# Kernel optimization log

Hardware: AMD Instinct MI355X
Metric: run time of the kernel (lower is better)

Reference implementation:

```python
import jax, jax.numpy as jnp
import numpy as np

DIM = 384
NUM_HEADS = 12
WS = 8            # window_size
SS = 4            # shift_size
HEAD_DIM = DIM // NUM_HEADS
SCALE = HEAD_DIM ** -0.5
N = WS * WS       # tokens per window
EPS = 1e-5
MLP_HIDDEN = 4 * DIM

# relative position index (static, matches torch buffer construction)
_coords = np.stack(np.meshgrid(np.arange(WS), np.arange(WS), indexing='ij')).reshape(2, -1)
_rel = (_coords[:, :, None] - _coords[:, None, :]).transpose(1, 2, 0)  # [N,N,2]
_rel[..., 0] += WS - 1
_rel[..., 1] += WS - 1
_rel[..., 0] *= 2 * WS - 1
RPI = jnp.asarray(_rel.sum(-1))  # [N,N] int


def layer_norm(x, g, b):
    m = x.mean(-1, keepdims=True)
    v = ((x - m) ** 2).mean(-1, keepdims=True)
    return (x - m) / jnp.sqrt(v + EPS) * g + b


def window_partition(x):
    B, Hh, Ww, C = x.shape
    x = x.reshape(B, Hh // WS, WS, Ww // WS, WS, C).transpose(0, 1, 3, 2, 4, 5)
    return x.reshape(-1, WS, WS, C)


def window_reverse(w, Hh, Ww):
    B = w.shape[0] // ((Hh // WS) * (Ww // WS))
    x = w.reshape(B, Hh // WS, Ww // WS, WS, WS, -1).transpose(0, 1, 3, 2, 4, 5)
    return x.reshape(B, Hh, Ww, -1)


def attention_mask(Hp, Wp):
    # region id along each axis: 0 = [0, Hp-WS), 1 = [Hp-WS, Hp-SS), 2 = [Hp-SS, Hp)
    h_id = np.zeros(Hp, np.int32); h_id[Hp - WS:Hp - SS] = 1; h_id[Hp - SS:] = 2
    w_id = np.zeros(Wp, np.int32); w_id[Wp - WS:Wp - SS] = 1; w_id[Wp - SS:] = 2
    cnt = h_id[:, None] * 3 + w_id[None, :]                      # [Hp, Wp]
    img = jnp.asarray(cnt, jnp.float32).reshape(1, Hp, Wp, 1)
    mw = window_partition(img).reshape(-1, N)                    # [nW, N]
    am = mw[:, None, :] - mw[:, :, None]                         # [nW, N, N]
    return jnp.where(am != 0, jnp.float32(-100.0), jnp.float32(0.0))


def setup_inputs() -> dict:
    key = jax.random.key(0)
    ks = jax.random.split(key, 8)
    B, H, W = 32, 64, 64
    std = 0.02
    return {
        'x': jax.random.normal(ks[0], (B, H * W, DIM), jnp.float32),
        'qkv_w': jax.random.normal(ks[1], (DIM, 3 * DIM), jnp.float32) * std,
        'qkv_b': jnp.zeros((3 * DIM,), jnp.float32),
        'proj_w': jax.random.normal(ks[2], (DIM, DIM), jnp.float32) * std,
        'proj_b': jnp.zeros((DIM,), jnp.float32),
        'rpb_table': jax.random.normal(ks[3], ((2 * WS - 1) * (2 * WS - 1), NUM_HEADS), jnp.float32) * std,
        'n1_g': jnp.ones((DIM,), jnp.float32), 'n1_b': jnp.zeros((DIM,), jnp.float32),
        'n2_g': jnp.ones((DIM,), jnp.float32), 'n2_b': jnp.zeros((DIM,), jnp.float32),
        'fc1_w': jax.random.normal(ks[4], (DIM, MLP_HIDDEN), jnp.float32) * std,
        'fc1_b': jnp.zeros((MLP_HIDDEN,), jnp.float32),
        'fc2_w': jax.random.normal(ks[5], (MLP_HIDDEN, DIM), jnp.float32) * std,
        'fc2_b': jnp.zeros((DIM,), jnp.float32),
        'H': 64, 'W': 64,
    }


def reference(x, qkv_w, qkv_b, proj_w, proj_b, rpb_table, n1_g, n1_b, n2_g, n2_b,
              fc1_w, fc1_b, fc2_w, fc2_b, H, W):
    B, L, C = x.shape
    shortcut = x
    h = layer_norm(x, n1_g, n1_b).reshape(B, H, W, C)
    pad_r = (WS - W % WS) % WS
    pad_b = (WS - H % WS) % WS
    if pad_r or pad_b:
        h = jnp.pad(h, ((0, 0), (0, pad_b), (0, pad_r), (0, 0)))
    Hp, Wp = H + pad_b, W + pad_r
    shifted = jnp.roll(h, shift=(-SS, -SS), axis=(1, 2))
    xw = window_partition(shifted).reshape(-1, N, C)             # [B_, N, C]
    B_ = xw.shape[0]

    qkv = (xw @ qkv_w + qkv_b).reshape(B_, N, 3, NUM_HEADS, HEAD_DIM)
    q = qkv[:, :, 0].transpose(0, 2, 1, 3) * SCALE               # [B_, h, N, d]
    k = qkv[:, :, 1].transpose(0, 2, 1, 3)
    v = qkv[:, :, 2].transpose(0, 2, 1, 3)

    attn = jnp.einsum('bhnd,bhmd->bhnm', q, k)                   # [B_, h, N, N]
    bias = rpb_table[RPI].transpose(2, 0, 1)                     # [h, N, N]
    attn = attn + bias[None]

    mask = attention_mask(Hp, Wp)                                # [nW, N, N]
    nW = mask.shape[0]
    attn = attn.reshape(B_ // nW, nW, NUM_HEADS, N, N) + mask[None, :, None]
    attn = jax.nn.softmax(attn.reshape(B_, NUM_HEADS, N, N), axis=-1)

    out = jnp.einsum('bhnm,bhmd->bhnd', attn, v)
    out = out.transpose(0, 2, 1, 3).reshape(B_, N, C)
    out = out @ proj_w + proj_b

    out = window_reverse(out.reshape(-1, WS, WS, C), Hp, Wp)
    out = jnp.roll(out, shift=(SS, SS), axis=(1, 2))
    out = out[:, :H, :W, :].reshape(B, H * W, C)

    x = shortcut + out
    h2 = layer_norm(x, n2_g, n2_b)
    mlp = jax.nn.gelu(h2 @ fc1_w + fc1_b, approximate=False) @ fc2_w + fc2_b
    return x + mlp
```

## Files before the change

### kernel.cpp

```cpp
#include <hip/hip_runtime.h>
#include <math.h>


#define ROWS_TOTAL 131072
#define NWIN_TOTAL 2048

typedef __attribute__((ext_vector_type(8))) __bf16 bf16x8;
typedef __attribute__((ext_vector_type(4))) float f32x4;
typedef __attribute__((ext_vector_type(8))) unsigned short ushort8;

__device__ __forceinline__ unsigned short f2bf(float f) {
  unsigned u = __builtin_bit_cast(unsigned, f);
  u = (u + 0x7fffu + ((u >> 16) & 1u)) >> 16;
  return (unsigned short)u;
}
__device__ __forceinline__ float bf2f(unsigned short u) {
  return __builtin_bit_cast(float, (unsigned)u << 16);
}

__device__ __forceinline__ void gload16(const void* g, void* l) {
  __builtin_amdgcn_global_load_lds(
      (const __attribute__((address_space(1))) unsigned int*)g,
      (__attribute__((address_space(3))) unsigned int*)l, 16, 0, 0);
}

__device__ __forceinline__ int gather_row(int win, int t) {
  int b = win >> 6, wi = (win >> 3) & 7, wj = win & 7;
  int gi = (wi * 8 + (t >> 3) + 4) & 63;
  int gj = (wj * 8 + (t & 7) + 4) & 63;
  return (b << 12) + (gi << 6) + gj;
}

__device__ __forceinline__ float gelu_f(float v) {
  float x = v * 0.70710678118654752f;
  float ax = fabsf(x);
  float t = 1.f / (1.f + 0.3275911f * ax);
  float poly =
      t * (0.254829592f +
           t * (-0.284496736f +
                t * (1.421413741f + t * (-1.453152027f + t * 1.061405429f))));
  float er = 1.f - poly * __expf(-x * x);
  er = copysignf(er, x);
  return 0.5f * v * (1.f + er);
}

#define VM4() asm volatile("s_waitcnt vmcnt(4)" ::: "memory")
#define VM0() asm volatile("s_waitcnt vmcnt(0)" ::: "memory")
#define ABAR() asm volatile("s_barrier" ::: "memory")

#define STGA_(buf_, kt_, c_)                                          \
  gload16(aSrcC[c_] + (size_t)(kt_) * 64,                             \
          (char*)As + (buf_) * 32768 + (c_) * 8192 + w * 1024)
#define STGB_(buf_, kt_, c_)                                          \
  gload16(bSrcC[c_] + (size_t)(kt_) * 64,                             \
          (char*)Bs + (buf_) * 24576 + (c_) * 8192 + w * 1024)

#define GEMM_DECLS()                                                  \
  f32x4 acc[8][3];                                                    \
  _Pragma("unroll") for (int i_ = 0; i_ < 8; ++i_)                    \
  _Pragma("unroll") for (int j_ = 0; j_ < 3; ++j_)                    \
      acc[i_][j_] = (f32x4)(0.f);                                     \
  const int sl0 = ((hi) ^ (lr & 7)) * 8;                              \
  const int sl1 = ((4 + hi) ^ (lr & 7)) * 8;                          \
  const int aB0 = (wr * 128 + lr) * 64 + sl0;                         \
  const int aB1 = (wr * 128 + lr) * 64 + sl1;                         \
  const int bB0 = (wc * 48 + lr) * 64 + sl0;                          \
  const int bB1 = (wc * 48 + lr) * 64 + sl1;

#define GEMM_CORE(NT_)                                                \
  {                                                                   \
    STGA_(0, 0, 0); STGA_(0, 0, 1); STGA_(0, 0, 2); STGA_(0, 0, 3);   \
    STGB_(0, 0, 0); STGB_(0, 0, 1); STGB_(0, 0, 2);                   \
    STGA_(1, 1, 0); STGA_(1, 1, 1); STGA_(1, 1, 2); STGA_(1, 1, 3);   \
    VM4(); ABAR();                                                    \
    int curA = 0;                                                     \
    for (int t = 0; t < (NT_); ++t) {                                 \
      const int curB = t & 1;                                         \
      const ushort* AsC = (const ushort*)As + curA * 16384;           \
      const ushort* BsC = (const ushort*)Bs + curB * 12288;           \
      if (t + 1 < (NT_)) {                                            \
        STGB_(curB ^ 1, t + 1, 0);                                    \
        STGB_(curB ^ 1, t + 1, 1);                                    \
        STGB_(curB ^ 1, t + 1, 2);                                    \
      }                                                               \
      if (t + 2 < (NT_)) {                                            \
        int nbA = curA + 2; if (nbA >= 3) nbA -= 3;                   \
        STGA_(nbA, t + 2, 0); STGA_(nbA, t + 2, 1);                   \
        STGA_(nbA, t + 2, 2); STGA_(nbA, t + 2, 3);                   \
      }                                                               \
      bf16x8 bv0[3], bv1[3];                                          \
      _Pragma("unroll") for (int nj = 0; nj < 3; ++nj) {              \
        bv0[nj] = *(const bf16x8*)(BsC + bB0 + nj * 1024);            \
        bv1[nj] = *(const bf16x8*)(BsC + bB1 + nj * 1024);            \
      }                                                               \
      _Pragma("unroll") for (int mi = 0; mi < 8; ++mi) {              \
        bf16x8 a0 = *(const bf16x8*)(AsC + aB0 + mi * 1024);          \
        bf16x8 a1 = *(const bf16x8*)(AsC + aB1 + mi * 1024);          \
        _Pragma("unroll") for (int nj = 0; nj < 3; ++nj) {            \
          acc[mi][nj] = __builtin_amdgcn_mfma_f32_16x16x32_bf16(      \
              a0, bv0[nj], acc[mi][nj], 0, 0, 0);                     \
          acc[mi][nj] = __builtin_amdgcn_mfma_f32_16x16x32_bf16(      \
              a1, bv1[nj], acc[mi][nj], 0, 0, 0);                     \
        }                                                             \
      }                                                               \
      if (t + 2 < (NT_)) { VM4(); ABAR(); }                           \
      else if (t + 1 < (NT_)) { VM0(); ABAR(); }                      \
      ++curA; if (curA == 3) curA = 0;                                \
    }                                                                 \
  }

#define GRID_SWZ(NP_)                                                 \
  int p, bm;                                                          \
  {                                                                   \
    int lin = blockIdx.y * (NP_) + blockIdx.x;                        \
    if ((gridDim.y & 7) == 0) {                                       \
      int xcd = lin & 7, q = lin >> 3;                                \
      p = q % (NP_); bm = (q / (NP_)) * 8 + xcd;                      \
    } else { p = blockIdx.x; bm = blockIdx.y; }                       \
  }

__global__ __launch_bounds__(256) void wprep_k(
    const float* __restrict__ qkvw, const float* __restrict__ projw,
    const float* __restrict__ fc1w, const float* __restrict__ fc2w,
    ushort* __restrict__ wq, ushort* __restrict__ wp,
    ushort* __restrict__ w1, ushort* __restrict__ w2) {
  int gid = blockIdx.x * 256 + threadIdx.x;
  const int S1 = 1152 * 384;
  const int S2 = S1 + 384 * 384;
  const int S3 = S2 + 1536 * 384;
  const int S4 = S3 + 384 * 1536;
  if (gid < S1) {
    int n = gid / 384, k = gid - n * 384;
    wq[gid] = f2bf(qkvw[(size_t)k * 1152 + n]);
  } else if (gid < S2) {
    int i = gid - S1, n = i / 384, k = i - n * 384;
    wp[i] = f2bf(projw[(size_t)k * 384 + n]);
  } else if (gid < S3) {
    int i = gid - S2, n = i / 384, k = i - n * 384;
    w1[i] = f2bf(fc1w[(size_t)k * 1536 + n]);
  } else if (gid < S4) {
    int i = gid - S3, n = i / 1536, k = i - n * 1536;
    w2[i] = f2bf(fc2w[(size_t)k * 384 + n]);
  }
}

__global__ __launch_bounds__(256) void ln_fused_k(
    const float* __restrict__ x, const float* __restrict__ g,
    const float* __restrict__ b, ushort* __restrict__ o) {
  int wid = threadIdx.x >> 6, lane = threadIdx.x & 63;
  int row = (blockIdx.x << 2) + wid;
  const float* p = x + (size_t)row * 384;
  float2 v[3];
  float s = 0.f, ss = 0.f;
#pragma unroll
  for (int c = 0; c < 3; ++c) {
    v[c] = *(const float2*)(p + lane * 2 + c * 128);
    s += v[c].x + v[c].y;
    ss += v[c].x * v[c].x + v[c].y * v[c].y;
  }
#pragma unroll
  for (int off = 1; off < 64; off <<= 1) {
    s += __shfl_xor(s, off);
    ss += __shfl_xor(ss, off);
  }
  float m = s * (1.f / 384.f);
  float r = rsqrtf(ss * (1.f / 384.f) - m * m + 1e-5f);
  ushort* op = o + (size_t)row * 384;
#pragma unroll
  for (int c = 0; c < 3; ++c) {
    float2 gg = *(const float2*)(g + lane * 2 + c * 128);
    float2 bb = *(const float2*)(b + lane * 2 + c * 128);
    union { ushort u[2]; unsigned w; } pk;
    pk.u[0] = f2bf((v[c].x - m) * r * gg.x + bb.x);
    pk.u[1] = f2bf((v[c].y - m) * r * gg.y + bb.y);
    *(unsigned*)(op + lane * 2 + c * 128) = pk.w;
  }
}

__global__ __launch_bounds__(512, 2) void qkv_mfma_k(
    const ushort* __restrict__ xln, const ushort* __restrict__ wq,
    const float* __restrict__ qkvb, ushort* __restrict__ qkvd, int wc0) {
  __shared__ __align__(16) ushort As[3][16384];
  __shared__ __align__(16) ushort Bs[2][12288];
  const int tid = threadIdx.x;
  const int w = tid >> 6, lane = tid & 63;
  const int wr = w >> 2, wc = w & 3;
  const int lr = lane & 15, hi = lane >> 4;
  GRID_SWZ(6);
  const int n0 = p * 192;
  const int sg = ((tid & 7) ^ ((tid >> 3) & 7)) * 8;
  const ushort* aSrcC[4];
  const ushort* bSrcC[3];
#pragma unroll
  for (int c = 0; c < 4; ++c)
    aSrcC[c] =
        xln + (size_t)gather_row(wc0 + bm * 4 + c, tid >> 3) * 384 + sg;
#pragma unroll
  for (int c = 0; c < 3; ++c)
    bSrcC[c] = wq + (size_t)(n0 + c * 64 + (tid >> 3)) * 384 + sg;
  GEMM_DECLS();
  GEMM_CORE(6);
  const float scale = 0.17677669529663687f;
#pragma unroll
  for (int mi = 0; mi < 8; ++mi) {
#pragma unroll
    for (int r = 0; r < 4; ++r) {
      int rr = wr * 128 + mi * 16 + (hi << 2) + r;
      size_t row = (size_t)(bm * 256 + rr);
#pragma unroll
      for (int nj = 0; nj < 3; ++nj) {
        int nc = n0 + wc * 48 + nj * 16 + lr;
        float v = acc[mi][nj][r] + qkvb[nc];
        if (nc < 384) v *= scale;
        qkvd[row * 1152 + nc] = f2bf(v);
      }
    }
  }
}

__global__ __launch_bounds__(128) void attn_k(
    const ushort* __restrict__ qkv, const float* __restrict__ rpb,
    ushort* __restrict__ ao, int wc0) {
  __shared__ __align__(16) float kbuf[2][64][32];
  __shared__ __align__(16) float vbuf[2][64][32];
  __shared__ float bias[2][232];
  __shared__ int region[64];
  const int tid = threadIdx.x;
  const int wid = tid >> 6, lane = tid & 63;
  const int w = blockIdx.x, win = wc0 + w;
  const int head = blockIdx.y * 2 + wid;
  if (tid < 64) {
    int wi = (win >> 3) & 7, wj = win & 7;
    int pi = wi * 8 + (tid >> 3), pj = wj * 8 + (tid & 7);
    int ri = pi < 56 ? 0 : (pi < 60 ? 1 : 2);
    int rj = pj < 56 ? 0 : (pj < 60 ? 1 : 2);
    region[tid] = ri * 3 + rj;
  }
  const ushort* base = qkv + (size_t)(w * 64) * 1152;
  const int kcol = 384 + head * 32, vcol = 768 + head * 32;
#pragma unroll
  for (int s = 0; s < 4; ++s) {
    int f = s * 64 + lane;
    int r = f >> 2, c = (f & 3) * 8;
    ushort8 ku = *(const ushort8*)(base + (size_t)r * 1152 + kcol + c);
    ushort8 vu = *(const ushort8*)(base + (size_t)r * 1152 + vcol + c);
#pragma unroll
    for (int j = 0; j < 8; ++j) {
      kbuf[wid][r][c + j] = bf2f(ku[j]);
      vbuf[wid][r][c + j] = bf2f(vu[j]);
    }
  }
  for (int s = lane; s < 225; s += 64) bias[wid][s] = rpb[s * 12 + head];
  __syncthreads();
  const int i = lane;
  float qr[32];
  const ushort* qp = base + (size_t)i * 1152 + head * 32;
#pragma unroll
  for (int c = 0; c < 4; ++c) {
    ushort8 qu = *(const ushort8*)(qp + c * 8);
#pragma unroll
    for (int j = 0; j < 8; ++j) qr[c * 8 + j] = bf2f(qu[j]);
  }
  const int yi = i >> 3, xi = i & 7, regi = region[i];
  float sc[64];
  float mx = -3.0e38f;
#pragma unroll
  for (int j = 0; j < 64; ++j) {
    float a = 0.f;
#pragma unroll
    for (int c = 0; c < 32; c += 4) {
      float4 kv = *(float4*)&kbuf[wid][j][c];
      a = fmaf(qr[c], kv.x, a);
      a = fmaf(qr[c + 1], kv.y, a);
      a = fmaf(qr[c + 2], kv.z, a);
      a = fmaf(qr[c + 3], kv.w, a);
    }
    int dy = yi - (j >> 3) + 7, dx = xi - (j & 7) + 7;
    a += bias[wid][dy * 15 + dx];
    if (region[j] != regi) a -= 100.f;
    sc[j] = a;
    mx = fmaxf(mx, a);
  }
  float sum = 0.f;
#pragma unroll
  for (int j = 0; j < 64; ++j) {
    float e = __expf(sc[j] - mx);
    sc[j] = e;
    sum += e;
  }
  const float inv = 1.f / sum;
  float o[32];
#pragma unroll
  for (int c = 0; c < 32; ++c) o[c] = 0.f;
#pragma unroll
  for (int j = 0; j < 64; ++j) {
    float p = sc[j];
#pragma unroll
    for (int c = 0; c < 32; c += 4) {
      float4 vv = *(float4*)&vbuf[wid][j][c];
      o[c] = fmaf(p, vv.x, o[c]);
      o[c + 1] = fmaf(p, vv.y, o[c + 1]);
      o[c + 2] = fmaf(p, vv.z, o[c + 2]);
      o[c + 3] = fmaf(p, vv.w, o[c + 3]);
    }
  }
  ushort* op = ao + ((size_t)(w * 64 + i)) * 384 + (head << 5);
#pragma unroll
  for (int c = 0; c < 32; c += 8) {
    ushort8 pk;
#pragma unroll
    for (int j2 = 0; j2 < 8; ++j2) pk[j2] = f2bf(o[c + j2] * inv);
    *(ushort8*)(op + c) = pk;
  }
}

__global__ __launch_bounds__(512, 2) void proj_mfma_k(
    const ushort* __restrict__ ao, const ushort* __restrict__ wp,
    const float* __restrict__ pb, const float* __restrict__ x,
    float* __restrict__ x2, int wc0) {
  __shared__ __align__(16) ushort As[3][16384];
  __shared__ __align__(16) ushort Bs[2][12288];
  const int tid = threadIdx.x;
  const int w = tid >> 6, lane = tid & 63;
  const int wr = w >> 2, wc = w & 3;
  const int lr = lane & 15, hi = lane >> 4;
  GRID_SWZ(2);
  const int n0 = p * 192;
  const int sg = ((tid & 7) ^ ((tid >> 3) & 7)) * 8;
  const ushort* aSrcC[4];
  const ushort* bSrcC[3];
#pragma unroll
  for (int c = 0; c < 4; ++c)
    aSrcC[c] = ao + (size_t)(bm * 256 + c * 64 + (tid >> 3)) * 384 + sg;
#pragma unroll
  for (int c = 0; c < 3; ++c)
    bSrcC[c] = wp + (size_t)(n0 + c * 64 + (tid >> 3)) * 384 + sg;
  GEMM_DECLS();
  GEMM_CORE(6);
#pragma unroll
  for (int mi = 0; mi < 8; ++mi) {
#pragma unroll
    for (int r = 0; r < 4; ++r) {
      int rr = wr * 128 + mi * 16 + (hi << 2) + r;
      int gl = bm * 256 + rr;
      int gr = gather_row(wc0 + (gl >> 6), gl & 63);
#pragma unroll
      for (int nj = 0; nj < 3; ++nj) {
        int nc = n0 + wc * 48 + nj * 16 + lr;
        size_t idx = (size_t)gr * 384 + nc;
        x2[idx] = acc[mi][nj][r] + pb[nc] + x[idx];
      }
    }
  }
}

__global__ __launch_bounds__(512, 2) void fc1_mfma_k(
    const ushort* __restrict__ x2ln, const ushort* __restrict__ w1,
    const float* __restrict__ fb, ushort* __restrict__ hm, int row0) {
  __shared__ __align__(16) ushort As[3][16384];
  __shared__ __align__(16) ushort Bs[2][12288];
  const int tid = threadIdx.x;
  const int w = tid >> 6, lane = tid & 63;
  const int wr = w >> 2, wc = w & 3;
  const int lr = lane & 15, hi = lane >> 4;
  GRID_SWZ(8);
  const int n0 = p * 192;
  const int sg = ((tid & 7) ^ ((tid >> 3) & 7)) * 8;
  const ushort* aSrcC[4];
  const ushort* bSrcC[3];
#pragma unroll
  for (int c = 0; c < 4; ++c)
    aSrcC[c] =
        x2ln + (size_t)(row0 + bm * 256 + c * 64 + (tid >> 3)) * 384 + sg;
#pragma unroll
  for (int c = 0; c < 3; ++c)
    bSrcC[c] = w1 + (size_t)(n0 + c * 64 + (tid >> 3)) * 384 + sg;
  GEMM_DECLS();
  GEMM_CORE(6);
#pragma unroll
  for (int mi = 0; mi < 8; ++mi) {
#pragma unroll
    for (int r = 0; r < 4; ++r) {
      int rr = wr * 128 + mi * 16 + (hi << 2) + r;
      size_t lrow = (size_t)(bm * 256 + rr);
#pragma unroll
      for (int nj = 0; nj < 3; ++nj) {
        int nc = n0 + wc * 48 + nj * 16 + lr;
        float v = gelu_f(acc[mi][nj][r] + fb[nc]);
        hm[lrow * 1536 + nc] = f2bf(v);
      }
    }
  }
}

__global__ __launch_bounds__(512, 2) void fc2_mfma_k(
    const ushort* __restrict__ hm, const ushort* __restrict__ w2,
    const float* __restrict__ fb, float* __restrict__ out, int row0) {
  __shared__ __align__(16) ushort As[3][16384];
  __shared__ __align__(16) ushort Bs[2][12288];
  const int tid = threadIdx.x;
  const int w = tid >> 6, lane = tid & 63;
  const int wr = w >> 2, wc = w & 3;
  const int lr = lane & 15, hi = lane >> 4;
  GRID_SWZ(2);
  const int n0 = p * 192;
  const int sg = ((tid & 7) ^ ((tid >> 3) & 7)) * 8;
  const ushort* aSrcC[4];
  const ushort* bSrcC[3];
#pragma unroll
  for (int c = 0; c < 4; ++c)
    aSrcC[c] = hm + (size_t)(bm * 256 + c * 64 + (tid >> 3)) * 1536 + sg;
#pragma unroll
  for (int c = 0; c < 3; ++c)
    bSrcC[c] = w2 + (size_t)(n0 + c * 64 + (tid >> 3)) * 1536 + sg;
  GEMM_DECLS();
  GEMM_CORE(24);
#pragma unroll
  for (int mi = 0; mi < 8; ++mi) {
#pragma unroll
    for (int r = 0; r < 4; ++r) {
      int rr = wr * 128 + mi * 16 + (hi << 2) + r;
      size_t grow = (size_t)(row0 + bm * 256 + rr);
#pragma unroll
      for (int nj = 0; nj < 3; ++nj) {
        int nc = n0 + wc * 48 + nj * 16 + lr;
        size_t idx = grow * 384 + nc;
        out[idx] = out[idx] + acc[mi][nj][r] + fb[nc];
      }
    }
  }
}

extern "C" void kernel_launch(void* const* d_in, const int* in_sizes, int n_in,
                              void* d_out, int out_size, void* d_ws, size_t ws_size,
                              hipStream_t stream) {
  const float* x = (const float*)d_in[0];
  const float* qkv_w = (const float*)d_in[1];
  const float* qkv_b = (const float*)d_in[2];
  const float* proj_w = (const float*)d_in[3];
  const float* proj_b = (const float*)d_in[4];
  const float* rpb = (const float*)d_in[5];
  const float* n1g = (const float*)d_in[6];
  const float* n1b = (const float*)d_in[7];
  const float* n2g = (const float*)d_in[8];
  const float* n2b = (const float*)d_in[9];
  const float* fc1w = (const float*)d_in[10];
  const float* fc1b = (const float*)d_in[11];
  const float* fc2w = (const float*)d_in[12];
  const float* fc2b = (const float*)d_in[13];
  float* out = (float*)d_out;
  char* ws = (char*)d_ws;

  ushort* wq = (ushort*)ws;
  ushort* wp = wq + 442368;
  ushort* w1 = wp + 147456;
  ushort* w2 = w1 + 589824;
  ushort* xln = (ushort*)(ws + 3538944);
  char* scratch = ws + 3538944 + 100663296;
  size_t base = 3538944 + 100663296;
  size_t ssz = (ws_size > base) ? ws_size - base : 0;

  wprep_k<<<6912, 256, 0, stream>>>(qkv_w, proj_w, fc1w, fc2w, wq, wp, w1, w2);
  ln_fused_k<<<ROWS_TOTAL / 4, 256, 0, stream>>>(x, n1g, n1b, xln);

  const size_t perwin = 196608;
  int nwc = (int)(ssz / perwin);
  if (nwc > NWIN_TOTAL) nwc = NWIN_TOTAL;
  nwc &= ~31;
  if (nwc < 32) nwc = 32;
  ushort* qkvd = (ushort*)scratch;
  ushort* ao = qkvd + (size_t)nwc * 73728;
  for (int wc0 = 0; wc0 < NWIN_TOTAL; wc0 += nwc) {
    int nw = (NWIN_TOTAL - wc0 < nwc) ? (NWIN_TOTAL - wc0) : nwc;
    qkv_mfma_k<<<dim3(6, nw / 4), 512, 0, stream>>>(xln, wq, qkv_b, qkvd, wc0);
    attn_k<<<dim3(nw, 6), 128, 0, stream>>>(qkvd, rpb, ao, wc0);
    proj_mfma_k<<<dim3(2, nw / 4), 512, 0, stream>>>(ao, wp, proj_b, x, out,
                                                     wc0);
  }

  ln_fused_k<<<ROWS_TOTAL / 4, 256, 0, stream>>>(out, n2g, n2b, xln);
  const size_t pergrp = 786432;
  int ngc = (int)(ssz / pergrp);
  if (ngc > 512) ngc = 512;
  ngc &= ~7;
  if (ngc < 8) ngc = 8;
  ushort* hm = (ushort*)scratch;
  for (int g0 = 0; g0 < 512; g0 += ngc) {
    int ng = (512 - g0 < ngc) ? (512 - g0) : ngc;
    fc1_mfma_k<<<dim3(8, ng), 512, 0, stream>>>(xln, w1, fc1b, hm, g0 * 256);
    fc2_mfma_k<<<dim3(2, ng), 512, 0, stream>>>(hm, w2, fc2b, out, g0 * 256);
  }
}
```

Before: 1.549 ms.

## Use weight-resident persistent GEMM kernels for QKV, proj and FC1

Replaces the QKV, projection and FC1 GEMMs with persistent 256-thread kernels. Each block keeps a 48-column weight panel (full K=384) resident in LDS and loops over 256-row M tiles with a stride of the grid height, double-buffering only the activation tiles. The aim is to stop re-streaming weight tiles for every output tile and to overlap the next tile's A load with the current epilogue. In exchange, per-block tiles are smaller (256x48) and the grid is capped, which may reduce MFMA density and occupancy. FC2 keeps its original kernel with the macros inlined.

```diff
diff --git a/kernel.cpp b/kernel.cpp
--- a/kernel.cpp
+++ b/kernel.cpp
@@ -48,75 +48,44 @@
 #define VM0() asm volatile("s_waitcnt vmcnt(0)" ::: "memory")
 #define ABAR() asm volatile("s_barrier" ::: "memory")
 
-#define STGA_(buf_, kt_, c_)                                          \
-  gload16(aSrcC[c_] + (size_t)(kt_) * 64,                             \
-          (char*)As + (buf_) * 32768 + (c_) * 8192 + w * 1024)
-#define STGB_(buf_, kt_, c_)                                          \
-  gload16(bSrcC[c_] + (size_t)(kt_) * 64,                             \
-          (char*)Bs + (buf_) * 24576 + (c_) * 8192 + w * 1024)
-
-#define GEMM_DECLS()                                                  \
-  f32x4 acc[8][3];                                                    \
-  _Pragma("unroll") for (int i_ = 0; i_ < 8; ++i_)                    \
-  _Pragma("unroll") for (int j_ = 0; j_ < 3; ++j_)                    \
-      acc[i_][j_] = (f32x4)(0.f);                                     \
-  const int sl0 = ((hi) ^ (lr & 7)) * 8;                              \
-  const int sl1 = ((4 + hi) ^ (lr & 7)) * 8;                          \
-  const int aB0 = (wr * 128 + lr) * 64 + sl0;                         \
-  const int aB1 = (wr * 128 + lr) * 64 + sl1;                         \
-  const int bB0 = (wc * 48 + lr) * 64 + sl0;                          \
-  const int bB1 = (wc * 48 + lr) * 64 + sl1;
-
-#define GEMM_CORE(NT_)                                                \
-  {                                                                   \
-    STGA_(0, 0, 0); STGA_(0, 0, 1); STGA_(0, 0, 2); STGA_(0, 0, 3);   \
-    STGB_(0, 0, 0); STGB_(0, 0, 1); STGB_(0, 0, 2);                   \
-    STGA_(1, 1, 0); STGA_(1, 1, 1); STGA_(1, 1, 2); STGA_(1, 1, 3);   \
-    VM4(); ABAR();                                                    \
-    int curA = 0;                                                     \
-    for (int t = 0; t < (NT_); ++t) {                                 \
-      const int curB = t & 1;                                         \
-      const ushort* AsC = (const ushort*)As + curA * 16384;           \
-      const ushort* BsC = (const ushort*)Bs + curB * 12288;           \
-      if (t + 1 < (NT_)) {                                            \
-        STGB_(curB ^ 1, t + 1, 0);                                    \
-        STGB_(curB ^ 1, t + 1, 1);                                    \
-        STGB_(curB ^ 1, t + 1, 2);                                    \
-      }                                                               \
-      if (t + 2 < (NT_)) {                                            \
-        int nbA = curA + 2; if (nbA >= 3) nbA -= 3;                   \
-        STGA_(nbA, t + 2, 0); STGA_(nbA, t + 2, 1);                   \
-        STGA_(nbA, t + 2, 2); STGA_(nbA, t + 2, 3);                   \
-      }                                                               \
-      bf16x8 bv0[3], bv1[3];                                          \
-      _Pragma("unroll") for (int nj = 0; nj < 3; ++nj) {              \
-        bv0[nj] = *(const bf16x8*)(BsC + bB0 + nj * 1024);            \
-        bv1[nj] = *(const bf16x8*)(BsC + bB1 + nj * 1024);            \
-      }                                                               \
-      _Pragma("unroll") for (int mi = 0; mi < 8; ++mi) {              \
-        bf16x8 a0 = *(const bf16x8*)(AsC + aB0 + mi * 1024);          \
-        bf16x8 a1 = *(const bf16x8*)(AsC + aB1 + mi * 1024);          \
-        _Pragma("unroll") for (int nj = 0; nj < 3; ++nj) {            \
-          acc[mi][nj] = __builtin_amdgcn_mfma_f32_16x16x32_bf16(      \
-              a0, bv0[nj], acc[mi][nj], 0, 0, 0);                     \
-          acc[mi][nj] = __builtin_amdgcn_mfma_f32_16x16x32_bf16(      \
-              a1, bv1[nj], acc[mi][nj], 0, 0, 0);                     \
-        }                                                             \
-      }                                                               \
-      if (t + 2 < (NT_)) { VM4(); ABAR(); }                           \
-      else if (t + 1 < (NT_)) { VM0(); ABAR(); }                      \
-      ++curA; if (curA == 3) curA = 0;                                \
-    }                                                                 \
-  }
-
-#define GRID_SWZ(NP_)                                                 \
-  int p, bm;                                                          \
-  {                                                                   \
-    int lin = blockIdx.y * (NP_) + blockIdx.x;                        \
-    if ((gridDim.y & 7) == 0) {                                       \
-      int xcd = lin & 7, q = lin >> 3;                                \
-      p = q % (NP_); bm = (q / (NP_)) * 8 + xcd;                      \
-    } else { p = blockIdx.x; bm = blockIdx.y; }                       \
+#define WSTG_A(buf_, kt_)                                               \
+  _Pragma("unroll") for (int c_ = 0; c_ < 4; ++c_)                      \
+      gload16(aSrc[c_] + (size_t)(kt_) * 64,                            \
+              (char*)As + (buf_) * 16384 + (c_ * 256 + tid) * 16);
+
+#define WGEMM_PRO()                                                     \
+  _Pragma("unroll") for (int i_ = 0; i_ < 9; ++i_) {                    \
+    int id_ = i_ * 256 + tid;                                           \
+    int row_ = id_ / 48, g_ = id_ - row_ * 48;                          \
+    gload16((const char*)bpan + (size_t)row_ * 768 +                    \
+                ((g_ ^ (row_ & 7)) << 4),                               \
+            (char*)Bres + id_ * 16);                                    \
+  }                                                                     \
+  int aOff[4], bRow[3];                                                 \
+  _Pragma("unroll") for (int mi_ = 0; mi_ < 4; ++mi_)                   \
+      aOff[mi_] = (w * 64 + mi_ * 16 + lr) * 64 +                       \
+                  ((hi ^ ((lr >> 1) & 3)) << 4);                        \
+  _Pragma("unroll") for (int nj_ = 0; nj_ < 3; ++nj_)                   \
+      bRow[nj_] = (nj_ * 16 + lr) * 768;                                \
+  const int sg = (((tid & 3) ^ ((tid >> 3) & 3)) << 4);
+
+#define WGEMM_STEP(t_, stage_, STAGE_EXPR)                              \
+  {                                                                     \
+    STAGE_EXPR;                                                         \
+    const int bslot = ((((t_) << 2) + hi) ^ (lr & 7)) << 4;             \
+    bf16x8 bv[3];                                                       \
+    _Pragma("unroll") for (int nj = 0; nj < 3; ++nj)                    \
+        bv[nj] = *(const bf16x8*)((char*)Bres + bRow[nj] + bslot);      \
+    _Pragma("unroll") for (int mi = 0; mi < 4; ++mi) {                  \
+      bf16x8 av =                                                       \
+          *(const bf16x8*)((char*)As + buf * 16384 + aOff[mi]);         \
+      _Pragma("unroll") for (int nj = 0; nj < 3; ++nj)                  \
+          acc[mi][nj] = __builtin_amdgcn_mfma_f32_16x16x32_bf16(        \
+              av, bv[nj], acc[mi][nj], 0, 0, 0);                        \
+    }                                                                   \
+    if (stage_) { VM4(); } else { VM0(); }                              \
+    ABAR();                                                             \
+    buf ^= 1;                                                           \
   }
 
 __global__ __launch_bounds__(256) void wprep_k(
@@ -177,45 +146,68 @@
   }
 }
 
-__global__ __launch_bounds__(512, 2) void qkv_mfma_k(
+__global__ __launch_bounds__(256) void qkv_wres_k(
     const ushort* __restrict__ xln, const ushort* __restrict__ wq,
-    const float* __restrict__ qkvb, ushort* __restrict__ qkvd, int wc0) {
-  __shared__ __align__(16) ushort As[3][16384];
-  __shared__ __align__(16) ushort Bs[2][12288];
+    const float* __restrict__ qkvb, ushort* __restrict__ qkvd, int wc0,
+    int NMT, int G) {
+  __shared__ __align__(16) ushort Bres[2304 * 8];
+  __shared__ __align__(16) ushort As[2][8192];
   const int tid = threadIdx.x;
-  const int w = tid >> 6, lane = tid & 63;
-  const int wr = w >> 2, wc = w & 3;
+  const int lane = tid & 63, w = tid >> 6;
   const int lr = lane & 15, hi = lane >> 4;
-  GRID_SWZ(6);
-  const int n0 = p * 192;
-  const int sg = ((tid & 7) ^ ((tid >> 3) & 7)) * 8;
-  const ushort* aSrcC[4];
-  const ushort* bSrcC[3];
-#pragma unroll
-  for (int c = 0; c < 4; ++c)
-    aSrcC[c] =
-        xln + (size_t)gather_row(wc0 + bm * 4 + c, tid >> 3) * 384 + sg;
-#pragma unroll
-  for (int c = 0; c < 3; ++c)
-    bSrcC[c] = wq + (size_t)(n0 + c * 64 + (tid >> 3)) * 384 + sg;
-  GEMM_DECLS();
-  GEMM_CORE(6);
+  const int p = blockIdx.x, n0 = p * 48;
+  const ushort* bpan = wq + (size_t)n0 * 384;
+  int mt = (int)blockIdx.y;
+  if (mt >= NMT) return;
+  WGEMM_PRO();
+  const char* aSrc[4];
+#define QKV_SETA(mt_)                                                   \
+  _Pragma("unroll") for (int c = 0; c < 4; ++c) {                       \
+    int rowc = (mt_) * 256 + c * 64 + (tid >> 2);                       \
+    aSrc[c] = (const char*)xln +                                        \
+              (size_t)gather_row(wc0 + (rowc >> 6), rowc & 63) * 768 +  \
+              sg;                                                       \
+  }
+  QKV_SETA(mt);
+  WSTG_A(0, 0);
+  VM0();
+  ABAR();
+  int buf = 0;
   const float scale = 0.17677669529663687f;
-#pragma unroll
-  for (int mi = 0; mi < 8; ++mi) {
-#pragma unroll
-    for (int r = 0; r < 4; ++r) {
-      int rr = wr * 128 + mi * 16 + (hi << 2) + r;
-      size_t row = (size_t)(bm * 256 + rr);
-#pragma unroll
-      for (int nj = 0; nj < 3; ++nj) {
-        int nc = n0 + wc * 48 + nj * 16 + lr;
-        float v = acc[mi][nj][r] + qkvb[nc];
-        if (nc < 384) v *= scale;
-        qkvd[row * 1152 + nc] = f2bf(v);
-      }
-    }
-  }
+  while (true) {
+    int nextmt = mt + G;
+    bool last = (nextmt >= NMT);
+    f32x4 acc[4][3];
+#pragma unroll
+    for (int i_ = 0; i_ < 4; ++i_)
+#pragma unroll
+      for (int j_ = 0; j_ < 3; ++j_) acc[i_][j_] = (f32x4)(0.f);
+    for (int t = 0; t < 11; ++t) {
+      WGEMM_STEP(t, true, WSTG_A(buf ^ 1, t + 1));
+    }
+    if (!last) {
+      WGEMM_STEP(11, true, { QKV_SETA(nextmt); WSTG_A(buf ^ 1, 0); });
+    } else {
+      WGEMM_STEP(11, false, {});
+    }
+#pragma unroll
+    for (int mi = 0; mi < 4; ++mi) {
+#pragma unroll
+      for (int r = 0; r < 4; ++r) {
+        size_t row = (size_t)(mt * 256 + w * 64 + mi * 16 + (hi << 2) + r);
+#pragma unroll
+        for (int nj = 0; nj < 3; ++nj) {
+          int nc = n0 + nj * 16 + lr;
+          float v = acc[mi][nj][r] + qkvb[nc];
+          if (nc < 384) v *= scale;
+          qkvd[row * 1152 + nc] = f2bf(v);
+        }
+      }
+    }
+    if (last) break;
+    mt = nextmt;
+  }
+#undef QKV_SETA
 }
 
 __global__ __launch_bounds__(128) void attn_k(
@@ -314,84 +306,133 @@
   }
 }
 
-__global__ __launch_bounds__(512, 2) void proj_mfma_k(
+__global__ __launch_bounds__(256) void proj_wres_k(
     const ushort* __restrict__ ao, const ushort* __restrict__ wp,
     const float* __restrict__ pb, const float* __restrict__ x,
-    float* __restrict__ x2, int wc0) {
-  __shared__ __align__(16) ushort As[3][16384];
-  __shared__ __align__(16) ushort Bs[2][12288];
+    float* __restrict__ x2, int wc0, int NMT, int G) {
+  __shared__ __align__(16) ushort Bres[2304 * 8];
+  __shared__ __align__(16) ushort As[2][8192];
   const int tid = threadIdx.x;
-  const int w = tid >> 6, lane = tid & 63;
-  const int wr = w >> 2, wc = w & 3;
+  const int lane = tid & 63, w = tid >> 6;
   const int lr = lane & 15, hi = lane >> 4;
-  GRID_SWZ(2);
-  const int n0 = p * 192;
-  const int sg = ((tid & 7) ^ ((tid >> 3) & 7)) * 8;
-  const ushort* aSrcC[4];
-  const ushort* bSrcC[3];
-#pragma unroll
-  for (int c = 0; c < 4; ++c)
-    aSrcC[c] = ao + (size_t)(bm * 256 + c * 64 + (tid >> 3)) * 384 + sg;
-#pragma unroll
-  for (int c = 0; c < 3; ++c)
-    bSrcC[c] = wp + (size_t)(n0 + c * 64 + (tid >> 3)) * 384 + sg;
-  GEMM_DECLS();
-  GEMM_CORE(6);
-#pragma unroll
-  for (int mi = 0; mi < 8; ++mi) {
-#pragma unroll
-    for (int r = 0; r < 4; ++r) {
-      int rr = wr * 128 + mi * 16 + (hi << 2) + r;
-      int gl = bm * 256 + rr;
-      int gr = gather_row(wc0 + (gl >> 6), gl & 63);
-#pragma unroll
-      for (int nj = 0; nj < 3; ++nj) {
-        int nc = n0 + wc * 48 + nj * 16 + lr;
-        size_t idx = (size_t)gr * 384 + nc;
-        x2[idx] = acc[mi][nj][r] + pb[nc] + x[idx];
-      }
-    }
-  }
-}
-
-__global__ __launch_bounds__(512, 2) void fc1_mfma_k(
+  const int p = blockIdx.x, n0 = p * 48;
+  const ushort* bpan = wp + (size_t)n0 * 384;
+  int mt = (int)blockIdx.y;
+  if (mt >= NMT) return;
+  WGEMM_PRO();
+  const char* aSrc[4];
+#define PROJ_SETA(mt_)                                                  \
+  _Pragma("unroll") for (int c = 0; c < 4; ++c)                         \
+      aSrc[c] = (const char*)ao +                                       \
+                (size_t)((mt_) * 256 + c * 64 + (tid >> 2)) * 768 + sg;
+  PROJ_SETA(mt);
+  WSTG_A(0, 0);
+  VM0();
+  ABAR();
+  int buf = 0;
+  while (true) {
+    int nextmt = mt + G;
+    bool last = (nextmt >= NMT);
+    f32x4 acc[4][3];
+#pragma unroll
+    for (int i_ = 0; i_ < 4; ++i_)
+#pragma unroll
+      for (int j_ = 0; j_ < 3; ++j_) acc[i_][j_] = (f32x4)(0.f);
+    for (int t = 0; t < 11; ++t) {
+      WGEMM_STEP(t, true, WSTG_A(buf ^ 1, t + 1));
+    }
+    if (!last) {
+      WGEMM_STEP(11, true, { PROJ_SETA(nextmt); WSTG_A(buf ^ 1, 0); });
+    } else {
+      WGEMM_STEP(11, false, {});
+    }
+#pragma unroll
+    for (int mi = 0; mi < 4; ++mi) {
+#pragma unroll
+      for (int r = 0; r < 4; ++r) {
+        int gl = mt * 256 + w * 64 + mi * 16 + (hi << 2) + r;
+        int gr = gather_row(wc0 + (gl >> 6), gl & 63);
+#pragma unroll
+        for (int nj = 0; nj < 3; ++nj) {
+          int nc = n0 + nj * 16 + lr;
+          size_t idx = (size_t)gr * 384 + nc;
+          x2[idx] = acc[mi][nj][r] + pb[nc] + x[idx];
+        }
+      }
+    }
+    if (last) break;
+    mt = nextmt;
+  }
+#undef PROJ_SETA
+}
+
+__global__ __launch_bounds__(256) void fc1_wres_k(
     const ushort* __restrict__ x2ln, const ushort* __restrict__ w1,
-    const float* __restrict__ fb, ushort* __restrict__ hm, int row0) {
-  __shared__ __align__(16) ushort As[3][16384];
-  __shared__ __align__(16) ushort Bs[2][12288];
+    const float* __restrict__ fb, ushort* __restrict__ hm, int row0,
+    int NMT, int G) {
+  __shared__ __align__(16) ushort Bres[2304 * 8];
+  __shared__ __align__(16) ushort As[2][8192];
   const int tid = threadIdx.x;
-  const int w = tid >> 6, lane = tid & 63;
-  const int wr = w >> 2, wc = w & 3;
+  const int lane = tid & 63, w = tid >> 6;
   const int lr = lane & 15, hi = lane >> 4;
-  GRID_SWZ(8);
-  const int n0 = p * 192;
-  const int sg = ((tid & 7) ^ ((tid >> 3) & 7)) * 8;
-  const ushort* aSrcC[4];
-  const ushort* bSrcC[3];
-#pragma unroll
-  for (int c = 0; c < 4; ++c)
-    aSrcC[c] =
-        x2ln + (size_t)(row0 + bm * 256 + c * 64 + (tid >> 3)) * 384 + sg;
-#pragma unroll
-  for (int c = 0; c < 3; ++c)
-    bSrcC[c] = w1 + (size_t)(n0 + c * 64 + (tid >> 3)) * 384 + sg;
-  GEMM_DECLS();
-  GEMM_CORE(6);
-#pragma unroll
-  for (int mi = 0; mi < 8; ++mi) {
-#pragma unroll
-    for (int r = 0; r < 4; ++r) {
-      int rr = wr * 128 + mi * 16 + (hi << 2) + r;
-      size_t lrow = (size_t)(bm * 256 + rr);
-#pragma unroll
-      for (int nj = 0; nj < 3; ++nj) {
-        int nc = n0 + wc * 48 + nj * 16 + lr;
-        float v = gelu_f(acc[mi][nj][r] + fb[nc]);
-        hm[lrow * 1536 + nc] = f2bf(v);
-      }
-    }
-  }
-}
+  const int p = blockIdx.x, n0 = p * 48;
+  const ushort* bpan = w1 + (size_t)n0 * 384;
+  int mt = (int)blockIdx.y;
+  if (mt >= NMT) return;
+  WGEMM_PRO();
+  const char* aSrc[4];
+#define FC1_SETA(mt_)                                                   \
+  _Pragma("unroll") for (int c = 0; c < 4; ++c)                         \
+      aSrc[c] = (const char*)x2ln +                                     \
+                (size_t)(row0 + (mt_) * 256 + c * 64 + (tid >> 2)) *    \
+                    768 +                                               \
+                sg;
+  FC1_SETA(mt);
+  WSTG_A(0, 0);
+  VM0();
+  ABAR();
+  int buf = 0;
+  while (true) {
+    int nextmt = mt + G;
+    bool last = (nextmt >= NMT);
+    f32x4 acc[4][3];
+#pragma unroll
+    for (int i_ = 0; i_ < 4; ++i_)
+#pragma unroll
+      for (int j_ = 0; j_ < 3; ++j_) acc[i_][j_] = (f32x4)(0.f);
+    for (int t = 0; t < 11; ++t) {
+      WGEMM_STEP(t, true, WSTG_A(buf ^ 1, t + 1));
+    }
+    if (!last) {
+      WGEMM_STEP(11, true, { FC1_SETA(nextmt); WSTG_A(buf ^ 1, 0); });
+    } else {
+      WGEMM_STEP(11, false, {});
+    }
+#pragma unroll
+    for (int mi = 0; mi < 4; ++mi) {
+#pragma unroll
+      for (int r = 0; r < 4; ++r) {
+        size_t lrow = (size_t)(mt * 256 + w * 64 + mi * 16 + (hi << 2) + r);
+#pragma unroll
+        for (int nj = 0; nj < 3; ++nj) {
+          int nc = n0 + nj * 16 + lr;
+          float v = gelu_f(acc[mi][nj][r] + fb[nc]);
+          hm[lrow * 1536 + nc] = f2bf(v);
+        }
+      }
+    }
+    if (last) break;
+    mt = nextmt;
+  }
+#undef FC1_SETA
+}
+
+#define STGA2_(buf_, kt_, c_)                                         \
+  gload16(aSrcC[c_] + (size_t)(kt_) * 64,                             \
+          (char*)As + (buf_) * 32768 + (c_) * 8192 + w * 1024)
+#define STGB2_(buf_, kt_, c_)                                         \
+  gload16(bSrcC[c_] + (size_t)(kt_) * 64,                             \
+          (char*)Bs + (buf_) * 24576 + (c_) * 8192 + w * 1024)
 
 __global__ __launch_bounds__(512, 2) void fc2_mfma_k(
     const ushort* __restrict__ hm, const ushort* __restrict__ w2,
@@ -402,19 +443,78 @@
   const int w = tid >> 6, lane = tid & 63;
   const int wr = w >> 2, wc = w & 3;
   const int lr = lane & 15, hi = lane >> 4;
-  GRID_SWZ(2);
+  int p, bm;
+  {
+    int lin = blockIdx.y * 2 + blockIdx.x;
+    if ((gridDim.y & 7) == 0) {
+      int xcd = lin & 7, q = lin >> 3;
+      p = q % 2; bm = (q / 2) * 8 + xcd;
+    } else { p = blockIdx.x; bm = blockIdx.y; }
+  }
   const int n0 = p * 192;
-  const int sg = ((tid & 7) ^ ((tid >> 3) & 7)) * 8;
+  const int sg2 = ((tid & 7) ^ ((tid >> 3) & 7)) * 8;
   const ushort* aSrcC[4];
   const ushort* bSrcC[3];
 #pragma unroll
   for (int c = 0; c < 4; ++c)
-    aSrcC[c] = hm + (size_t)(bm * 256 + c * 64 + (tid >> 3)) * 1536 + sg;
+    aSrcC[c] = hm + (size_t)(bm * 256 + c * 64 + (tid >> 3)) * 1536 + sg2;
 #pragma unroll
   for (int c = 0; c < 3; ++c)
-    bSrcC[c] = w2 + (size_t)(n0 + c * 64 + (tid >> 3)) * 1536 + sg;
-  GEMM_DECLS();
-  GEMM_CORE(24);
+    bSrcC[c] = w2 + (size_t)(n0 + c * 64 + (tid >> 3)) * 1536 + sg2;
+  f32x4 acc[8][3];
+#pragma unroll
+  for (int i_ = 0; i_ < 8; ++i_)
+#pragma unroll
+    for (int j_ = 0; j_ < 3; ++j_) acc[i_][j_] = (f32x4)(0.f);
+  const int sl0 = ((hi) ^ (lr & 7)) * 8;
+  const int sl1 = ((4 + hi) ^ (lr & 7)) * 8;
+  const int aB0 = (wr * 128 + lr) * 64 + sl0;
+  const int aB1 = (wr * 128 + lr) * 64 + sl1;
+  const int bB0 = (wc * 48 + lr) * 64 + sl0;
+  const int bB1 = (wc * 48 + lr) * 64 + sl1;
+  {
+    STGA2_(0, 0, 0); STGA2_(0, 0, 1); STGA2_(0, 0, 2); STGA2_(0, 0, 3);
+    STGB2_(0, 0, 0); STGB2_(0, 0, 1); STGB2_(0, 0, 2);
+    STGA2_(1, 1, 0); STGA2_(1, 1, 1); STGA2_(1, 1, 2); STGA2_(1, 1, 3);
+    VM4(); ABAR();
+    int curA = 0;
+    for (int t = 0; t < 24; ++t) {
+      const int curB = t & 1;
+      const ushort* AsC = (const ushort*)As + curA * 16384;
+      const ushort* BsC = (const ushort*)Bs + curB * 12288;
+      if (t + 1 < 24) {
+        STGB2_(curB ^ 1, t + 1, 0);
+        STGB2_(curB ^ 1, t + 1, 1);
+        STGB2_(curB ^ 1, t + 1, 2);
+      }
+      if (t + 2 < 24) {
+        int nbA = curA + 2; if (nbA >= 3) nbA -= 3;
+        STGA2_(nbA, t + 2, 0); STGA2_(nbA, t + 2, 1);
+        STGA2_(nbA, t + 2, 2); STGA2_(nbA, t + 2, 3);
+      }
+      bf16x8 bv0[3], bv1[3];
+#pragma unroll
+      for (int nj = 0; nj < 3; ++nj) {
+        bv0[nj] = *(const bf16x8*)(BsC + bB0 + nj * 1024);
+        bv1[nj] = *(const bf16x8*)(BsC + bB1 + nj * 1024);
+      }
+#pragma unroll
+      for (int mi = 0; mi < 8; ++mi) {
+        bf16x8 a0 = *(const bf16x8*)(AsC + aB0 + mi * 1024);
+        bf16x8 a1 = *(const bf16x8*)(AsC + aB1 + mi * 1024);
+#pragma unroll
+        for (int nj = 0; nj < 3; ++nj) {
+          acc[mi][nj] = __builtin_amdgcn_mfma_f32_16x16x32_bf16(
+              a0, bv0[nj], acc[mi][nj], 0, 0, 0);
+          acc[mi][nj] = __builtin_amdgcn_mfma_f32_16x16x32_bf16(
+              a1, bv1[nj], acc[mi][nj], 0, 0, 0);
+        }
+      }
+      if (t + 2 < 24) { VM4(); ABAR(); }
+      else if (t + 1 < 24) { VM0(); ABAR(); }
+      ++curA; if (curA == 3) curA = 0;
+    }
+  }
 #pragma unroll
   for (int mi = 0; mi < 8; ++mi) {
 #pragma unroll
@@ -472,10 +572,14 @@
   ushort* ao = qkvd + (size_t)nwc * 73728;
   for (int wc0 = 0; wc0 < NWIN_TOTAL; wc0 += nwc) {
     int nw = (NWIN_TOTAL - wc0 < nwc) ? (NWIN_TOTAL - wc0) : nwc;
-    qkv_mfma_k<<<dim3(6, nw / 4), 512, 0, stream>>>(xln, wq, qkv_b, qkvd, wc0);
+    int NMT = nw / 4;
+    int Gq = NMT < 24 ? NMT : 24;
+    int Gp = NMT < 64 ? NMT : 64;
+    qkv_wres_k<<<dim3(24, Gq), 256, 0, stream>>>(xln, wq, qkv_b, qkvd, wc0,
+                                                 NMT, Gq);
     attn_k<<<dim3(nw, 6), 128, 0, stream>>>(qkvd, rpb, ao, wc0);
-    proj_mfma_k<<<dim3(2, nw / 4), 512, 0, stream>>>(ao, wp, proj_b, x, out,
-                                                     wc0);
+    proj_wres_k<<<dim3(8, Gp), 256, 0, stream>>>(ao, wp, proj_b, x, out, wc0,
+                                                 NMT, Gp);
   }
 
   ln_fused_k<<<ROWS_TOTAL / 4, 256, 0, stream>>>(out, n2g, n2b, xln);
@@ -487,7 +591,9 @@
   ushort* hm = (ushort*)scratch;
   for (int g0 = 0; g0 < 512; g0 += ngc) {
     int ng = (512 - g0 < ngc) ? (512 - g0) : ngc;
-    fc1_mfma_k<<<dim3(8, ng), 512, 0, stream>>>(xln, w1, fc1b, hm, g0 * 256);
+    int G1 = ng < 16 ? ng : 16;
+    fc1_wres_k<<<dim3(32, G1), 256, 0, stream>>>(xln, w1, fc1b, hm, g0 * 256,
+                                                 ng, G1);
     fc2_mfma_k<<<dim3(2, ng), 512, 0, stream>>>(hm, w2, fc2b, out, g0 * 256);
   }
 }
```

New measurement: 1.822 ms. 17.7% more time.
